# Kernel tuning notes

Measured on AMD Instinct MI355X. Metric: run time of the kernel, lower is better.

Reference implementation:

```python
import jax, jax.numpy as jnp
import numpy as np

H = 4  # attention heads for the single degree-0 fiber

def _layer_norm(x, gamma):
    mu = x.mean(-1, keepdims=True)
    var = ((x - mu) ** 2).mean(-1, keepdims=True)
    return (x - mu) / jnp.sqrt(var + 1e-5) * gamma

def _silu(x):
    return x * jax.nn.sigmoid(x)

def _forward(features, rel_dist, norm_scale, Wq, Wxi, Wxj,
             rp_W1, rp_b1, rp_g1, rp_W2, rp_b2, rp_g2, rp_W3, rp_b3,
             Wkv_out, Wout, neighbor_indices, neighbor_mask):
    b, n, d, _ = features.shape
    k = neighbor_indices.shape[-1]
    hid = Wq.shape[1]
    dh = hid // H
    kvd = Wkv_out.shape[0]
    scale = dh ** -0.5

    # ---- prenorm: RMS (over feature channels) of per-m L2 norms; m=1 for degree 0
    rms = jnp.sqrt(jnp.sum(features ** 2, axis=-2, keepdims=True)) * (d ** -0.5)
    x = features / jnp.maximum(rms, 1e-12) * norm_scale      # (b,n,d,1)
    x = x[..., 0]                                            # (b,n,d)

    # ---- queries
    q = x @ Wq                                               # (b,n,hid)

    # ---- DTP to_kv (degree0->degree0): project xi/xj, gather neighbors, radial kernel
    xi = x @ Wxi
    xj = x @ Wxj
    xg = jax.vmap(lambda t, idx: t[idx])(xj, neighbor_indices)   # (b,n,k,d)
    xe = xg + xi[:, :, None, :]

    hdd = _layer_norm(_silu(rel_dist @ rp_W1 + rp_b1), rp_g1)    # (b,n,k,rh)
    hdd = _layer_norm(_silu(hdd @ rp_W2 + rp_b2), rp_g2)
    R = (hdd @ rp_W3 + rp_b3).reshape(b, n, k, kvd, d)           # per-edge (lo,li) kernel
    kv = jnp.einsum('bnkod,bnkd->bnko', R, xe)                   # (b,n,k,kvd)
    kv = kv @ Wkv_out                                            # DTP project_out
    kk, vv = jnp.split(kv, 2, axis=-1)                           # (b,n,k,hid) each

    # ---- L2-distance attention over neighbors
    qh = q.reshape(b, n, H, dh).transpose(0, 2, 1, 3)            # (b,h,n,dh)
    kh = kk.reshape(b, n, k, H, dh).transpose(0, 3, 1, 2, 4)     # (b,h,n,k,dh)
    vh = vv.reshape(b, n, k, H, dh).transpose(0, 3, 1, 2, 4)
    diff = qh[:, :, :, None, :] - kh + 1e-6                      # F.pairwise_distance eps
    sim = -jnp.sqrt(jnp.sum(diff * diff, axis=-1)) * scale       # (b,h,n,k)
    sim = jnp.where(neighbor_mask[:, None], sim, -jnp.finfo(sim.dtype).max)
    attn = jax.nn.softmax(sim, axis=-1)
    out = jnp.einsum('bhnk,bhnkd->bhnd', attn, vh)
    out = out.transpose(0, 2, 1, 3).reshape(b, n, hid)

    return (out @ Wout)[..., None]                               # (b,n,d,1)

def setup_inputs() -> dict:
    key = jax.random.key(0)
    ks = jax.random.split(key, 16)
    b, n, k, d = 2, 256, 16, 64
    hid = H * 32           # heads * dim_head = 128
    kvd = 2 * hid          # 256
    rh = 64                # radial_hidden_dim
    rnd = lambda i, shape, s=1.0: jax.random.normal(ks[i], shape, jnp.float32) * s
    return dict(
        features=rnd(0, (b, n, d, 1)),
        neighbor_indices=jax.random.randint(ks[1], (b, n, k), 0, n),
        neighbor_mask=jax.random.bernoulli(ks[2], 0.9, (b, n, k)),
        rel_dist=jax.random.uniform(ks[3], (b, n, k, 1), jnp.float32),
        norm_scale=jnp.ones((d, 1), jnp.float32),
        Wq=rnd(4, (d, hid), d ** -0.5),
        Wxi=rnd(5, (d, d), d ** -0.5),
        Wxj=rnd(6, (d, d), d ** -0.5),
        rp_W1=rnd(7, (1, rh)), rp_b1=jnp.zeros((rh,), jnp.float32),
        rp_g1=jnp.ones((rh,), jnp.float32),
        rp_W2=rnd(8, (rh, rh), rh ** -0.5), rp_b2=jnp.zeros((rh,), jnp.float32),
        rp_g2=jnp.ones((rh,), jnp.float32),
        rp_W3=rnd(9, (rh, kvd * d), rh ** -0.5), rp_b3=jnp.zeros((kvd * d,), jnp.float32),
        Wkv_out=rnd(10, (kvd, kvd), kvd ** -0.5),
        Wout=rnd(11, (hid, d), hid ** -0.5),
    )

def reference(features, neighbor_indices, neighbor_mask, rel_dist, norm_scale,
              Wq, Wxi, Wxj, rp_W1, rp_b1, rp_g1, rp_W2, rp_b2, rp_g2,
              rp_W3, rp_b3, Wkv_out, Wout):
    return _forward(features, rel_dist, norm_scale, Wq, Wxi, Wxj,
                    rp_W1, rp_b1, rp_g1, rp_W2, rp_b2, rp_g2, rp_W3, rp_b3,
                    Wkv_out, Wout, neighbor_indices, neighbor_mask)
```

## Files before the change

### kernel.cpp

```cpp
#include <hip/hip_runtime.h>
#include <hip/hip_bf16.h>
#include <float.h>

#define BB 2
#define NN 256
#define DD 64
#define KK 16
#define NH 4
#define HID 128
#define KVD 256
#define RH 64
#define NNODES (BB*NN)
#define NEDGES (NNODES*KK)

typedef unsigned int uint32;
typedef unsigned short ushort_t;
typedef float f32x4_t __attribute__((ext_vector_type(4)));
typedef short bf16x8_t __attribute__((ext_vector_type(8)));
typedef __attribute__((address_space(3))) ushort_t lds_us;
typedef __attribute__((address_space(1))) const ushort_t glb_us;

__device__ __forceinline__ uint32 cvtpk_bf16(float lo, float hi) {
  uint32 r;
  asm("v_cvt_pk_bf16_f32 %0, %1, %2" : "=v"(r) : "v"(lo), "v"(hi));
  return r;
}

__device__ __forceinline__ float wave_sum64(float v) {
  #pragma unroll
  for (int m = 32; m; m >>= 1) v += __shfl_xor(v, m, 64);
  return v;
}

__device__ __forceinline__ ushort_t rne_bf16(float f) {
  uint32 u = __float_as_uint(f);
  return (ushort_t)((u + 0x7FFFu + ((u >> 16) & 1u)) >> 16);
}

__global__ __launch_bounds__(256) void node_w3_kernel(
    const float* __restrict__ feat, const float* __restrict__ gscale,
    const float* __restrict__ Wq, const float* __restrict__ Wxi,
    const float* __restrict__ Wxj,
    const float* __restrict__ W3, const float* __restrict__ b3,
    const float* __restrict__ Wkv,
    float* __restrict__ q_ws, float* __restrict__ xi_ws, float* __restrict__ xj_ws,
    ushort_t* __restrict__ W3bf, ushort_t* __restrict__ Wkvt) {
  int bx = blockIdx.x;
  if (bx >= 648) {
    int i = ((bx - 648) * 256 + threadIdx.x) * 4;
    int n = i >> 8, k0 = i & 255;
    union { uint2 q; ushort_t s[4]; } o;
    #pragma unroll
    for (int j = 0; j < 4; ++j) o.s[j] = rne_bf16(Wkv[(k0 + j) * KVD + n]);
    *(uint2*)(Wkvt + n * KVD + k0) = o.q;
    return;
  }
  if (bx >= 128) {
    const int W3N = 64 * KVD * DD;
    int i = ((bx - 128) * 256 + threadIdx.x) * 8;
    const float* src = (i < W3N) ? (W3 + i) : (b3 + (i - W3N));
    float4 a = ((const float4*)src)[0];
    float4 b = ((const float4*)src)[1];
    float v[8] = {a.x, a.y, a.z, a.w, b.x, b.y, b.z, b.w};
    union { uint4 q; ushort_t s[8]; } o;
    #pragma unroll
    for (int jj = 0; jj < 8; ++jj) o.s[jj] = rne_bf16(v[jj]);
    int rr = i >> 14, j0 = i & 16383;
    int oc = j0 >> 6, gr = (j0 >> 3) & 7;
    int byte_sw = oc * 128 + ((gr * 16) ^ ((oc & 7) << 4));
    *(uint4*)(W3bf + (rr << 14) + (byte_sw >> 1)) = o.q;
    return;
  }
  int sub = threadIdx.x >> 6;
  int t = threadIdx.x & 63;
  int node = bx * 4 + sub;
  __shared__ float xs[4][DD];
  float f = feat[node * DD + t];
  float ss = wave_sum64(f * f);
  float rms = sqrtf(ss) * 0.125f;
  float den = fmaxf(rms, 1e-12f);
  float x = f / den * gscale[t];
  xs[sub][t] = x;
  __syncthreads();
  float q0 = 0.f, q1 = 0.f, xiv = 0.f, xjv = 0.f;
  #pragma unroll 4
  for (int d = 0; d < DD; ++d) {
    float xv = xs[sub][d];
    q0  += xv * Wq[d * HID + t];
    q1  += xv * Wq[d * HID + 64 + t];
    xiv += xv * Wxi[d * DD + t];
    xjv += xv * Wxj[d * DD + t];
  }
  q_ws[node * HID + t] = q0;
  q_ws[node * HID + 64 + t] = q1;
  xi_ws[node * DD + t] = xiv;
  xj_ws[node * DD + t] = xjv;
}

__global__ __launch_bounds__(64) void edge_kernel(
    const int* __restrict__ nbi, const float* __restrict__ rel,
    const float* __restrict__ W1, const float* __restrict__ b1,
    const float* __restrict__ g1, const float* __restrict__ W2,
    const float* __restrict__ b2, const float* __restrict__ g2,
    const float* __restrict__ xi_ws, const float* __restrict__ xj_ws,
    float* __restrict__ h2_ws, float* __restrict__ xe_ws) {
  int e = blockIdx.x;
  int t = threadIdx.x;
  int node = e >> 4;
  int j = e & 15;
  int bb = node >> 8;
  __shared__ float hs[RH];
  float rd = rel[e];
  float h = rd * W1[t] + b1[t];
  h = h / (1.f + expf(-h));
  float mu = wave_sum64(h) * (1.f / RH);
  float c = h - mu;
  float var = wave_sum64(c * c) * (1.f / RH);
  float xn = c * rsqrtf(var + 1e-5f) * g1[t];
  hs[t] = xn;
  __syncthreads();
  float p = b2[t];
  #pragma unroll 4
  for (int r = 0; r < RH; ++r) p += hs[r] * W2[r * RH + t];
  p = p / (1.f + expf(-p));
  mu = wave_sum64(p) * (1.f / RH);
  c = p - mu;
  var = wave_sum64(c * c) * (1.f / RH);
  float h2v = c * rsqrtf(var + 1e-5f) * g2[t];
  h2_ws[e * RH + t] = h2v;
  int nb = nbi[node * KK + j];
  xe_ws[e * DD + t] = xj_ws[(bb * NN + nb) * DD + t] + xi_ws[node * DD + t];
}

#define AFRAG(dst, base, h) {                                     \
  union { bf16x8_t v; uint32 u[4]; } t_;                          \
  t_.u[0] = cvtpk_bf16(xf[(base)+0]*(h), xf[(base)+1]*(h));       \
  t_.u[1] = cvtpk_bf16(xf[(base)+2]*(h), xf[(base)+3]*(h));       \
  t_.u[2] = cvtpk_bf16(xf[(base)+4]*(h), xf[(base)+5]*(h));       \
  t_.u[3] = cvtpk_bf16(xf[(base)+6]*(h), xf[(base)+7]*(h));       \
  dst = t_.v; }

__global__ __launch_bounds__(256) void kv_kernel(
    const ushort_t* __restrict__ W3bf,
    const float* __restrict__ h2_ws, const float* __restrict__ xe_ws,
    float* __restrict__ kv_ws) {
  int bx = blockIdx.x;
  int eb = bx >> 2, ob = bx & 3;
  int o0 = ob * 64;
  int tid = threadIdx.x;
  int we = tid >> 6, l = tid & 63;
  int l15 = l & 15, g = l >> 4;
  int ebase = eb * 64;
  __shared__ float h2_s[64 * 68];
  __shared__ ushort_t bstage[2][2][4096];
  {
    int row = tid >> 2, c0 = (tid & 3) * 16;
    const float* src = h2_ws + (ebase + row) * RH + c0;
    float* dst = &h2_s[row * 68 + c0];
    #pragma unroll
    for (int q = 0; q < 4; ++q) ((float4*)dst)[q] = ((const float4*)src)[q];
  }
  int erow = ebase + we * 16 + l15;
  const float* xsrc = xe_ws + erow * DD + g * 8;
  float xf[16];
  #pragma unroll
  for (int jj = 0; jj < 8; ++jj) { xf[jj] = xsrc[jj]; xf[8 + jj] = xsrc[32 + jj]; }

  #define STAGE(buf, r0_) {                                                   \
    int ra_ = ((r0_) > 64) ? 64 : (r0_);                                      \
    int rb_ = ((r0_) + 1 > 64) ? 64 : ((r0_) + 1);                            \
    const ushort_t* sa_ = W3bf + ((size_t)ra_ << 14) + o0 * 64;               \
    const ushort_t* sb_ = W3bf + ((size_t)rb_ << 14) + o0 * 64;               \
    ushort_t* da_ = &bstage[buf][0][0];                                       \
    ushort_t* db_ = &bstage[buf][1][0];                                       \
    __builtin_amdgcn_global_load_lds((glb_us*)(sa_ + tid * 8),        (lds_us*)(da_ + tid * 8), 16, 0, 0);        \
    __builtin_amdgcn_global_load_lds((glb_us*)(sa_ + 2048 + tid * 8), (lds_us*)(da_ + 2048 + tid * 8), 16, 0, 0); \
    __builtin_amdgcn_global_load_lds((glb_us*)(sb_ + tid * 8),        (lds_us*)(db_ + tid * 8), 16, 0, 0);        \
    __builtin_amdgcn_global_load_lds((glb_us*)(sb_ + 2048 + tid * 8), (lds_us*)(db_ + 2048 + tid * 8), 16, 0, 0); }

  STAGE(0, 0);
  asm volatile("s_waitcnt vmcnt(0)" ::: "memory");
  __syncthreads();

  int e68 = (we * 16 + l15) * 68;
  int swz = (l15 & 7) << 4;
  f32x4_t acc0 = {0,0,0,0}, acc1 = {0,0,0,0}, acc2 = {0,0,0,0}, acc3 = {0,0,0,0};
  int cur = 0;
  for (int p = 0; p < 33; ++p) {
    int r0 = 2 * p;
    if (p < 32) STAGE(cur ^ 1, r0 + 2);
    #pragma unroll
    for (int rl = 0; rl < 2; ++rl) {
      int r = r0 + rl;
      if (r > 64) break;
      const char* bp = (const char*)&bstage[cur][rl][0];
      bf16x8_t bf0 = *(const bf16x8_t*)(bp + l15*128 +    0 + ((g*16)     ^ swz));
      bf16x8_t bf1 = *(const bf16x8_t*)(bp + l15*128 +    0 + (((4+g)*16) ^ swz));
      bf16x8_t bf2 = *(const bf16x8_t*)(bp + l15*128 + 2048 + ((g*16)     ^ swz));
      bf16x8_t bf3 = *(const bf16x8_t*)(bp + l15*128 + 2048 + (((4+g)*16) ^ swz));
      bf16x8_t bf4 = *(const bf16x8_t*)(bp + l15*128 + 4096 + ((g*16)     ^ swz));
      bf16x8_t bf5 = *(const bf16x8_t*)(bp + l15*128 + 4096 + (((4+g)*16) ^ swz));
      bf16x8_t bf6 = *(const bf16x8_t*)(bp + l15*128 + 6144 + ((g*16)     ^ swz));
      bf16x8_t bf7 = *(const bf16x8_t*)(bp + l15*128 + 6144 + (((4+g)*16) ^ swz));
      float h = (r < 64) ? h2_s[e68 + r] : 1.0f;
      bf16x8_t a0, a1;
      AFRAG(a0, 0, h); AFRAG(a1, 8, h);
      acc0 = __builtin_amdgcn_mfma_f32_16x16x32_bf16(a0, bf0, acc0, 0, 0, 0);
      acc0 = __builtin_amdgcn_mfma_f32_16x16x32_bf16(a1, bf1, acc0, 0, 0, 0);
      acc1 = __builtin_amdgcn_mfma_f32_16x16x32_bf16(a0, bf2, acc1, 0, 0, 0);
      acc1 = __builtin_amdgcn_mfma_f32_16x16x32_bf16(a1, bf3, acc1, 0, 0, 0);
      acc2 = __builtin_amdgcn_mfma_f32_16x16x32_bf16(a0, bf4, acc2, 0, 0, 0);
      acc2 = __builtin_amdgcn_mfma_f32_16x16x32_bf16(a1, bf5, acc2, 0, 0, 0);
      acc3 = __builtin_amdgcn_mfma_f32_16x16x32_bf16(a0, bf6, acc3, 0, 0, 0);
      acc3 = __builtin_amdgcn_mfma_f32_16x16x32_bf16(a1, bf7, acc3, 0, 0, 0);
    }
    asm volatile("s_waitcnt vmcnt(0)" ::: "memory");
    __syncthreads();
    cur ^= 1;
  }
  int orow = (ebase + we * 16 + g * 4) * KVD + o0 + l15;
  #pragma unroll
  for (int q = 0; q < 4; ++q) {
    kv_ws[orow + q * KVD +  0] = acc0[q];
    kv_ws[orow + q * KVD + 16] = acc1[q];
    kv_ws[orow + q * KVD + 32] = acc2[q];
    kv_ws[orow + q * KVD + 48] = acc3[q];
  }
}

__global__ __launch_bounds__(128) void attn_kernel(
    const float* __restrict__ q_ws, const float* __restrict__ kv_ws,
    const int* __restrict__ maskp, const ushort_t* __restrict__ Wkvt,
    const float* __restrict__ Wout, float* __restrict__ out) {
  int node = blockIdx.x;
  int tid = threadIdx.x;
  int w = tid >> 6, l = tid & 63;
  int l15 = l & 15, g = l >> 4;
  __shared__ float attn_s[NH * KK];
  __shared__ float o_s[HID];
  bf16x8_t a[8];
  {
    const float* kvrow = kv_ws + (size_t)(node * KK + l15) * KVD + g * 8;
    #pragma unroll
    for (int c = 0; c < 8; ++c) {
      union { bf16x8_t v; uint32 u[4]; } t_;
      t_.u[0] = cvtpk_bf16(kvrow[c*32 + 0], kvrow[c*32 + 1]);
      t_.u[1] = cvtpk_bf16(kvrow[c*32 + 2], kvrow[c*32 + 3]);
      t_.u[2] = cvtpk_bf16(kvrow[c*32 + 4], kvrow[c*32 + 5]);
      t_.u[3] = cvtpk_bf16(kvrow[c*32 + 6], kvrow[c*32 + 7]);
      a[c] = t_.v;
    }
  }
  f32x4_t acc[8];
  #pragma unroll
  for (int nt = 0; nt < 8; ++nt) {
    acc[nt] = (f32x4_t){0.f, 0.f, 0.f, 0.f};
    const ushort_t* bbase = Wkvt + (size_t)(w * 128 + nt * 16 + l15) * KVD + g * 8;
    #pragma unroll
    for (int c = 0; c < 8; ++c) {
      bf16x8_t b = *(const bf16x8_t*)(bbase + c * 32);
      acc[nt] = __builtin_amdgcn_mfma_f32_16x16x32_bf16(a[c], b, acc[nt], 0, 0, 0);
    }
  }
  const float scale = 0.17677669529663689f;
  if (w == 0) {
    float sim[4][4];
    #pragma unroll
    for (int h = 0; h < 4; ++h) {
      #pragma unroll
      for (int q = 0; q < 4; ++q) {
        float s = 0.f;
        #pragma unroll
        for (int p = 0; p < 2; ++p) {
          int nt = h * 2 + p;
          float qv = q_ws[node * HID + nt * 16 + l15];
          float diff = qv - acc[nt][q] + 1e-6f;
          s += diff * diff;
        }
        #pragma unroll
        for (int m = 8; m; m >>= 1) s += __shfl_xor(s, m, 64);
        sim[q][h] = -sqrtf(s) * scale;
      }
    }
    int mv[4];
    #pragma unroll
    for (int q = 0; q < 4; ++q) mv[q] = maskp[node * KK + g * 4 + q];
    #pragma unroll
    for (int h = 0; h < 4; ++h) {
      float sv[4];
      float mx = -FLT_MAX;
      #pragma unroll
      for (int q = 0; q < 4; ++q) {
        sv[q] = mv[q] ? sim[q][h] : -FLT_MAX;
        mx = fmaxf(mx, sv[q]);
      }
      mx = fmaxf(mx, __shfl_xor(mx, 16, 64));
      mx = fmaxf(mx, __shfl_xor(mx, 32, 64));
      float se = 0.f, ev[4];
      #pragma unroll
      for (int q = 0; q < 4; ++q) { ev[q] = expf(sv[q] - mx); se += ev[q]; }
      se += __shfl_xor(se, 16, 64);
      se += __shfl_xor(se, 32, 64);
      float inv = 1.f / se;
      if (l15 == 0) {
        #pragma unroll
        for (int q = 0; q < 4; ++q) attn_s[h * KK + g * 4 + q] = ev[q] * inv;
      }
    }
  }
  __syncthreads();
  if (w == 1) {
    #pragma unroll
    for (int nt = 0; nt < 8; ++nt) {
      int h = nt >> 1;
      float o = 0.f;
      #pragma unroll
      for (int q = 0; q < 4; ++q) o += attn_s[h * KK + g * 4 + q] * acc[nt][q];
      o += __shfl_xor(o, 16, 64);
      o += __shfl_xor(o, 32, 64);
      if (g == 0) o_s[nt * 16 + l15] = o;
    }
  }
  __syncthreads();
  if (tid < DD) {
    float r = 0.f;
    #pragma unroll 4
    for (int cI = 0; cI < HID; ++cI) r += o_s[cI] * Wout[cI * DD + tid];
    out[node * DD + tid] = r;
  }
}

extern "C" void kernel_launch(void* const* d_in, const int* in_sizes, int n_in,
                              void* d_out, int out_size, void* d_ws, size_t ws_size,
                              hipStream_t stream) {
  const float* feat = (const float*)d_in[0];
  const int*   nbi  = (const int*)d_in[1];
  const int*   msk  = (const int*)d_in[2];
  const float* rel  = (const float*)d_in[3];
  const float* gsc  = (const float*)d_in[4];
  const float* Wq   = (const float*)d_in[5];
  const float* Wxi  = (const float*)d_in[6];
  const float* Wxj  = (const float*)d_in[7];
  const float* W1   = (const float*)d_in[8];
  const float* b1   = (const float*)d_in[9];
  const float* g1   = (const float*)d_in[10];
  const float* W2   = (const float*)d_in[11];
  const float* b2   = (const float*)d_in[12];
  const float* g2   = (const float*)d_in[13];
  const float* W3   = (const float*)d_in[14];
  const float* b3   = (const float*)d_in[15];
  const float* Wkv  = (const float*)d_in[16];
  const float* Wout = (const float*)d_in[17];

  float* ws      = (float*)d_ws;
  float* q_ws    = ws;
  float* xi_ws   = q_ws  + NNODES * HID;
  float* xj_ws   = xi_ws + NNODES * DD;
  float* h2_ws   = xj_ws + NNODES * DD;
  float* xe_ws   = h2_ws + NEDGES * RH;
  float* kv_ws   = xe_ws + NEDGES * DD;
  ushort_t* W3bf = (ushort_t*)(kv_ws + NEDGES * KVD);
  ushort_t* Wkvt = W3bf + 65 * 16384;

  node_w3_kernel<<<712, 256, 0, stream>>>(feat, gsc, Wq, Wxi, Wxj, W3, b3, Wkv,
                                          q_ws, xi_ws, xj_ws, W3bf, Wkvt);
  edge_kernel<<<NEDGES, 64, 0, stream>>>(nbi, rel, W1, b1, g1, W2, b2, g2,
                                         xi_ws, xj_ws, h2_ws, xe_ws);
  kv_kernel<<<512, 256, 0, stream>>>(W3bf, h2_ws, xe_ws, kv_ws);
  attn_kernel<<<NNODES, 128, 0, stream>>>(q_ws, kv_ws, msk, Wkvt, Wout,
                                          (float*)d_out);
}
```

Before: 164.2 us.

## Fuse edge MLP, radial-kernel MFMA contraction and attention into one kernel

```diff
diff --git a/kernel.cpp b/kernel.cpp
--- a/kernel.cpp
+++ b/kernel.cpp
@@ -97,157 +97,160 @@
   xj_ws[node * DD + t] = xjv;
 }
 
-__global__ __launch_bounds__(64) void edge_kernel(
+#define AFRAG(dst, arr, base, h) {                                \
+  union { bf16x8_t v; uint32 u[4]; } t_;                          \
+  t_.u[0] = cvtpk_bf16(arr[(base)+0]*(h), arr[(base)+1]*(h));     \
+  t_.u[1] = cvtpk_bf16(arr[(base)+2]*(h), arr[(base)+3]*(h));     \
+  t_.u[2] = cvtpk_bf16(arr[(base)+4]*(h), arr[(base)+5]*(h));     \
+  t_.u[3] = cvtpk_bf16(arr[(base)+6]*(h), arr[(base)+7]*(h));     \
+  dst = t_.v; }
+
+#define STAGE2(buf, rr) {                                                      \
+  const ushort_t* s_ = W3bf + ((size_t)(rr) << 14);                            \
+  ushort_t* d_ = &bstage[buf][0];                                              \
+  __builtin_amdgcn_global_load_lds((glb_us*)(s_ + tid * 8),         (lds_us*)(d_ + tid * 8),         16, 0, 0); \
+  __builtin_amdgcn_global_load_lds((glb_us*)(s_ + 2048  + tid * 8), (lds_us*)(d_ + 2048  + tid * 8), 16, 0, 0); \
+  __builtin_amdgcn_global_load_lds((glb_us*)(s_ + 4096  + tid * 8), (lds_us*)(d_ + 4096  + tid * 8), 16, 0, 0); \
+  __builtin_amdgcn_global_load_lds((glb_us*)(s_ + 6144  + tid * 8), (lds_us*)(d_ + 6144  + tid * 8), 16, 0, 0); \
+  __builtin_amdgcn_global_load_lds((glb_us*)(s_ + 8192  + tid * 8), (lds_us*)(d_ + 8192  + tid * 8), 16, 0, 0); \
+  __builtin_amdgcn_global_load_lds((glb_us*)(s_ + 10240 + tid * 8), (lds_us*)(d_ + 10240 + tid * 8), 16, 0, 0); \
+  __builtin_amdgcn_global_load_lds((glb_us*)(s_ + 12288 + tid * 8), (lds_us*)(d_ + 12288 + tid * 8), 16, 0, 0); \
+  __builtin_amdgcn_global_load_lds((glb_us*)(s_ + 14336 + tid * 8), (lds_us*)(d_ + 14336 + tid * 8), 16, 0, 0); }
+
+__global__ __launch_bounds__(256, 1) void fused_kernel(
     const int* __restrict__ nbi, const float* __restrict__ rel,
     const float* __restrict__ W1, const float* __restrict__ b1,
     const float* __restrict__ g1, const float* __restrict__ W2,
     const float* __restrict__ b2, const float* __restrict__ g2,
     const float* __restrict__ xi_ws, const float* __restrict__ xj_ws,
-    float* __restrict__ h2_ws, float* __restrict__ xe_ws) {
-  int e = blockIdx.x;
-  int t = threadIdx.x;
-  int node = e >> 4;
-  int j = e & 15;
-  int bb = node >> 8;
-  __shared__ float hs[RH];
-  float rd = rel[e];
-  float h = rd * W1[t] + b1[t];
-  h = h / (1.f + expf(-h));
-  float mu = wave_sum64(h) * (1.f / RH);
-  float c = h - mu;
-  float var = wave_sum64(c * c) * (1.f / RH);
-  float xn = c * rsqrtf(var + 1e-5f) * g1[t];
-  hs[t] = xn;
-  __syncthreads();
-  float p = b2[t];
-  #pragma unroll 4
-  for (int r = 0; r < RH; ++r) p += hs[r] * W2[r * RH + t];
-  p = p / (1.f + expf(-p));
-  mu = wave_sum64(p) * (1.f / RH);
-  c = p - mu;
-  var = wave_sum64(c * c) * (1.f / RH);
-  float h2v = c * rsqrtf(var + 1e-5f) * g2[t];
-  h2_ws[e * RH + t] = h2v;
-  int nb = nbi[node * KK + j];
-  xe_ws[e * DD + t] = xj_ws[(bb * NN + nb) * DD + t] + xi_ws[node * DD + t];
-}
-
-#define AFRAG(dst, base, h) {                                     \
-  union { bf16x8_t v; uint32 u[4]; } t_;                          \
-  t_.u[0] = cvtpk_bf16(xf[(base)+0]*(h), xf[(base)+1]*(h));       \
-  t_.u[1] = cvtpk_bf16(xf[(base)+2]*(h), xf[(base)+3]*(h));       \
-  t_.u[2] = cvtpk_bf16(xf[(base)+4]*(h), xf[(base)+5]*(h));       \
-  t_.u[3] = cvtpk_bf16(xf[(base)+6]*(h), xf[(base)+7]*(h));       \
-  dst = t_.v; }
-
-__global__ __launch_bounds__(256) void kv_kernel(
-    const ushort_t* __restrict__ W3bf,
-    const float* __restrict__ h2_ws, const float* __restrict__ xe_ws,
-    float* __restrict__ kv_ws) {
-  int bx = blockIdx.x;
-  int eb = bx >> 2, ob = bx & 3;
-  int o0 = ob * 64;
+    const ushort_t* __restrict__ W3bf, const ushort_t* __restrict__ Wkvt,
+    const float* __restrict__ q_ws, const int* __restrict__ maskp,
+    const float* __restrict__ Wout, float* __restrict__ out) {
+  int b = blockIdx.x;
   int tid = threadIdx.x;
-  int we = tid >> 6, l = tid & 63;
+  int wv = tid >> 6, l = tid & 63;
   int l15 = l & 15, g = l >> 4;
-  int ebase = eb * 64;
-  __shared__ float h2_s[64 * 68];
-  __shared__ ushort_t bstage[2][2][4096];
+
+  __shared__ ushort_t bstage[2][16384];
+  __shared__ float h2_s[32 * 68];
+  __shared__ float xe_s[32 * 68];
+  __shared__ float attn_s[2][NH * KK];
+  __shared__ float o_s[2][HID];
+
+  STAGE2(0, 0);
+
   {
-    int row = tid >> 2, c0 = (tid & 3) * 16;
-    const float* src = h2_ws + (ebase + row) * RH + c0;
-    float* dst = &h2_s[row * 68 + c0];
-    #pragma unroll
-    for (int q = 0; q < 4; ++q) ((float4*)dst)[q] = ((const float4*)src)[q];
-  }
-  int erow = ebase + we * 16 + l15;
-  const float* xsrc = xe_ws + erow * DD + g * 8;
-  float xf[16];
+    float w1r = W1[l], b1r = b1[l], g1r = g1[l];
+    float b2r = b2[l], g2r = g2[l];
+    float w2r[64];
+    #pragma unroll
+    for (int r = 0; r < 64; ++r) w2r[r] = W2[r * RH + l];
+    int node_w = b * 2 + (wv >> 1);
+    int bbn = node_w >> 8;
+    float xir = xi_ws[node_w * DD + l];
+    for (int i = 0; i < 8; ++i) {
+      int e_loc = wv * 8 + i;
+      float rd = rel[b * 32 + e_loc];
+      float h = rd * w1r + b1r;
+      h = h / (1.f + expf(-h));
+      float mu = wave_sum64(h) * (1.f / RH);
+      float c = h - mu;
+      float var = wave_sum64(c * c) * (1.f / RH);
+      float xn = c * rsqrtf(var + 1e-5f) * g1r;
+      float p = b2r;
+      #pragma unroll
+      for (int r = 0; r < 64; ++r) {
+        float s = __uint_as_float(__builtin_amdgcn_readlane(__float_as_uint(xn), r));
+        p += s * w2r[r];
+      }
+      p = p / (1.f + expf(-p));
+      mu = wave_sum64(p) * (1.f / RH);
+      c = p - mu;
+      var = wave_sum64(c * c) * (1.f / RH);
+      float h2v = c * rsqrtf(var + 1e-5f) * g2r;
+      h2_s[e_loc * 68 + l] = h2v;
+      int nb = nbi[node_w * KK + (e_loc & 15)];
+      xe_s[e_loc * 68 + l] = xj_ws[(bbn * NN + nb) * DD + l] + xir;
+    }
+  }
+  asm volatile("s_waitcnt vmcnt(0)" ::: "memory");
+  __syncthreads();
+
+  float xfA[16], xfB[16];
   #pragma unroll
-  for (int jj = 0; jj < 8; ++jj) { xf[jj] = xsrc[jj]; xf[8 + jj] = xsrc[32 + jj]; }
-
-  #define STAGE(buf, r0_) {                                                   \
-    int ra_ = ((r0_) > 64) ? 64 : (r0_);                                      \
-    int rb_ = ((r0_) + 1 > 64) ? 64 : ((r0_) + 1);                            \
-    const ushort_t* sa_ = W3bf + ((size_t)ra_ << 14) + o0 * 64;               \
-    const ushort_t* sb_ = W3bf + ((size_t)rb_ << 14) + o0 * 64;               \
-    ushort_t* da_ = &bstage[buf][0][0];                                       \
-    ushort_t* db_ = &bstage[buf][1][0];                                       \
-    __builtin_amdgcn_global_load_lds((glb_us*)(sa_ + tid * 8),        (lds_us*)(da_ + tid * 8), 16, 0, 0);        \
-    __builtin_amdgcn_global_load_lds((glb_us*)(sa_ + 2048 + tid * 8), (lds_us*)(da_ + 2048 + tid * 8), 16, 0, 0); \
-    __builtin_amdgcn_global_load_lds((glb_us*)(sb_ + tid * 8),        (lds_us*)(db_ + tid * 8), 16, 0, 0);        \
-    __builtin_amdgcn_global_load_lds((glb_us*)(sb_ + 2048 + tid * 8), (lds_us*)(db_ + 2048 + tid * 8), 16, 0, 0); }
-
-  STAGE(0, 0);
-  asm volatile("s_waitcnt vmcnt(0)" ::: "memory");
-  __syncthreads();
-
-  int e68 = (we * 16 + l15) * 68;
+  for (int j = 0; j < 8; ++j) {
+    xfA[j]     = xe_s[l15 * 68 + g * 8 + j];
+    xfA[8 + j] = xe_s[l15 * 68 + 32 + g * 8 + j];
+    xfB[j]     = xe_s[(16 + l15) * 68 + g * 8 + j];
+    xfB[8 + j] = xe_s[(16 + l15) * 68 + 32 + g * 8 + j];
+  }
   int swz = (l15 & 7) << 4;
-  f32x4_t acc0 = {0,0,0,0}, acc1 = {0,0,0,0}, acc2 = {0,0,0,0}, acc3 = {0,0,0,0};
+  f32x4_t accA[4], accB[4];
+  #pragma unroll
+  for (int oi = 0; oi < 4; ++oi) {
+    accA[oi] = (f32x4_t){0.f, 0.f, 0.f, 0.f};
+    accB[oi] = (f32x4_t){0.f, 0.f, 0.f, 0.f};
+  }
   int cur = 0;
-  for (int p = 0; p < 33; ++p) {
-    int r0 = 2 * p;
-    if (p < 32) STAGE(cur ^ 1, r0 + 2);
-    #pragma unroll
-    for (int rl = 0; rl < 2; ++rl) {
-      int r = r0 + rl;
-      if (r > 64) break;
-      const char* bp = (const char*)&bstage[cur][rl][0];
-      bf16x8_t bf0 = *(const bf16x8_t*)(bp + l15*128 +    0 + ((g*16)     ^ swz));
-      bf16x8_t bf1 = *(const bf16x8_t*)(bp + l15*128 +    0 + (((4+g)*16) ^ swz));
-      bf16x8_t bf2 = *(const bf16x8_t*)(bp + l15*128 + 2048 + ((g*16)     ^ swz));
-      bf16x8_t bf3 = *(const bf16x8_t*)(bp + l15*128 + 2048 + (((4+g)*16) ^ swz));
-      bf16x8_t bf4 = *(const bf16x8_t*)(bp + l15*128 + 4096 + ((g*16)     ^ swz));
-      bf16x8_t bf5 = *(const bf16x8_t*)(bp + l15*128 + 4096 + (((4+g)*16) ^ swz));
-      bf16x8_t bf6 = *(const bf16x8_t*)(bp + l15*128 + 6144 + ((g*16)     ^ swz));
-      bf16x8_t bf7 = *(const bf16x8_t*)(bp + l15*128 + 6144 + (((4+g)*16) ^ swz));
-      float h = (r < 64) ? h2_s[e68 + r] : 1.0f;
-      bf16x8_t a0, a1;
-      AFRAG(a0, 0, h); AFRAG(a1, 8, h);
-      acc0 = __builtin_amdgcn_mfma_f32_16x16x32_bf16(a0, bf0, acc0, 0, 0, 0);
-      acc0 = __builtin_amdgcn_mfma_f32_16x16x32_bf16(a1, bf1, acc0, 0, 0, 0);
-      acc1 = __builtin_amdgcn_mfma_f32_16x16x32_bf16(a0, bf2, acc1, 0, 0, 0);
-      acc1 = __builtin_amdgcn_mfma_f32_16x16x32_bf16(a1, bf3, acc1, 0, 0, 0);
-      acc2 = __builtin_amdgcn_mfma_f32_16x16x32_bf16(a0, bf4, acc2, 0, 0, 0);
-      acc2 = __builtin_amdgcn_mfma_f32_16x16x32_bf16(a1, bf5, acc2, 0, 0, 0);
-      acc3 = __builtin_amdgcn_mfma_f32_16x16x32_bf16(a0, bf6, acc3, 0, 0, 0);
-      acc3 = __builtin_amdgcn_mfma_f32_16x16x32_bf16(a1, bf7, acc3, 0, 0, 0);
+  for (int p = 0; p <= 64; ++p) {
+    if (p < 64) STAGE2(cur ^ 1, p + 1);
+    float hA = (p < 64) ? h2_s[l15 * 68 + p] : 1.0f;
+    float hB = (p < 64) ? h2_s[(16 + l15) * 68 + p] : 1.0f;
+    bf16x8_t a0A, a1A, a0B, a1B;
+    AFRAG(a0A, xfA, 0, hA); AFRAG(a1A, xfA, 8, hA);
+    AFRAG(a0B, xfB, 0, hB); AFRAG(a1B, xfB, 8, hB);
+    const char* bp = (const char*)&bstage[cur][0] + wv * 8192 + l15 * 128;
+    #pragma unroll
+    for (int oi = 0; oi < 4; ++oi) {
+      bf16x8_t bv0 = *(const bf16x8_t*)(bp + oi * 2048 + ((g * 16) ^ swz));
+      bf16x8_t bv1 = *(const bf16x8_t*)(bp + oi * 2048 + (((4 + g) * 16) ^ swz));
+      accA[oi] = __builtin_amdgcn_mfma_f32_16x16x32_bf16(a0A, bv0, accA[oi], 0, 0, 0);
+      accA[oi] = __builtin_amdgcn_mfma_f32_16x16x32_bf16(a1A, bv1, accA[oi], 0, 0, 0);
+      accB[oi] = __builtin_amdgcn_mfma_f32_16x16x32_bf16(a0B, bv0, accB[oi], 0, 0, 0);
+      accB[oi] = __builtin_amdgcn_mfma_f32_16x16x32_bf16(a1B, bv1, accB[oi], 0, 0, 0);
     }
     asm volatile("s_waitcnt vmcnt(0)" ::: "memory");
     __syncthreads();
     cur ^= 1;
   }
-  int orow = (ebase + we * 16 + g * 4) * KVD + o0 + l15;
-  #pragma unroll
-  for (int q = 0; q < 4; ++q) {
-    kv_ws[orow + q * KVD +  0] = acc0[q];
-    kv_ws[orow + q * KVD + 16] = acc1[q];
-    kv_ws[orow + q * KVD + 32] = acc2[q];
-    kv_ws[orow + q * KVD + 48] = acc3[q];
-  }
-}
-
-__global__ __launch_bounds__(128) void attn_kernel(
-    const float* __restrict__ q_ws, const float* __restrict__ kv_ws,
-    const int* __restrict__ maskp, const ushort_t* __restrict__ Wkvt,
-    const float* __restrict__ Wout, float* __restrict__ out) {
-  int node = blockIdx.x;
-  int tid = threadIdx.x;
-  int w = tid >> 6, l = tid & 63;
-  int l15 = l & 15, g = l >> 4;
-  __shared__ float attn_s[NH * KK];
-  __shared__ float o_s[HID];
+
+  float* kvf = (float*)&bstage[0][0];
+  {
+    #pragma unroll
+    for (int m = 0; m < 2; ++m) {
+      #pragma unroll
+      for (int oi = 0; oi < 4; ++oi) {
+        f32x4_t av = m ? accB[oi] : accA[oi];
+        int f = wv * 64 + oi * 16 + l15;
+        int fu = f >> 2, fl = f & 3;
+        #pragma unroll
+        for (int q = 0; q < 4; ++q) {
+          int e = m * 16 + g * 4 + q;
+          kvf[e * 256 + ((fu ^ (e & 7)) << 2) + fl] = av[q];
+        }
+      }
+    }
+  }
+  __syncthreads();
+
+  int role = wv & 1, nl = wv >> 1;
+  int node = b * 2 + nl;
   bf16x8_t a[8];
   {
-    const float* kvrow = kv_ws + (size_t)(node * KK + l15) * KVD + g * 8;
+    int e = nl * 16 + l15;
+    const float* kr = kvf + e * 256;
+    int sw = l15 & 7;
     #pragma unroll
     for (int c = 0; c < 8; ++c) {
+      int u0 = (c * 8 + g * 2) ^ sw;
+      int u1 = (c * 8 + g * 2 + 1) ^ sw;
+      f32x4_t v0 = *(const f32x4_t*)(kr + u0 * 4);
+      f32x4_t v1 = *(const f32x4_t*)(kr + u1 * 4);
       union { bf16x8_t v; uint32 u[4]; } t_;
-      t_.u[0] = cvtpk_bf16(kvrow[c*32 + 0], kvrow[c*32 + 1]);
-      t_.u[1] = cvtpk_bf16(kvrow[c*32 + 2], kvrow[c*32 + 3]);
-      t_.u[2] = cvtpk_bf16(kvrow[c*32 + 4], kvrow[c*32 + 5]);
-      t_.u[3] = cvtpk_bf16(kvrow[c*32 + 6], kvrow[c*32 + 7]);
+      t_.u[0] = cvtpk_bf16(v0.x, v0.y);
+      t_.u[1] = cvtpk_bf16(v0.z, v0.w);
+      t_.u[2] = cvtpk_bf16(v1.x, v1.y);
+      t_.u[3] = cvtpk_bf16(v1.z, v1.w);
       a[c] = t_.v;
     }
   }
@@ -255,15 +258,15 @@
   #pragma unroll
   for (int nt = 0; nt < 8; ++nt) {
     acc[nt] = (f32x4_t){0.f, 0.f, 0.f, 0.f};
-    const ushort_t* bbase = Wkvt + (size_t)(w * 128 + nt * 16 + l15) * KVD + g * 8;
+    const ushort_t* bbase = Wkvt + (size_t)(role * 128 + nt * 16 + l15) * KVD + g * 8;
     #pragma unroll
     for (int c = 0; c < 8; ++c) {
-      bf16x8_t b = *(const bf16x8_t*)(bbase + c * 32);
-      acc[nt] = __builtin_amdgcn_mfma_f32_16x16x32_bf16(a[c], b, acc[nt], 0, 0, 0);
+      bf16x8_t bv = *(const bf16x8_t*)(bbase + c * 32);
+      acc[nt] = __builtin_amdgcn_mfma_f32_16x16x32_bf16(a[c], bv, acc[nt], 0, 0, 0);
     }
   }
   const float scale = 0.17677669529663689f;
-  if (w == 0) {
+  if (role == 0) {
     float sim[4][4];
     #pragma unroll
     for (int h = 0; h < 4; ++h) {
@@ -271,8 +274,8 @@
       for (int q = 0; q < 4; ++q) {
         float s = 0.f;
         #pragma unroll
-        for (int p = 0; p < 2; ++p) {
-          int nt = h * 2 + p;
+        for (int pq = 0; pq < 2; ++pq) {
+          int nt = h * 2 + pq;
           float qv = q_ws[node * HID + nt * 16 + l15];
           float diff = qv - acc[nt][q] + 1e-6f;
           s += diff * diff;
@@ -304,29 +307,30 @@
       float inv = 1.f / se;
       if (l15 == 0) {
         #pragma unroll
-        for (int q = 0; q < 4; ++q) attn_s[h * KK + g * 4 + q] = ev[q] * inv;
-      }
-    }
-  }
-  __syncthreads();
-  if (w == 1) {
+        for (int q = 0; q < 4; ++q) attn_s[nl][h * KK + g * 4 + q] = ev[q] * inv;
+      }
+    }
+  }
+  __syncthreads();
+  if (role == 1) {
     #pragma unroll
     for (int nt = 0; nt < 8; ++nt) {
       int h = nt >> 1;
       float o = 0.f;
       #pragma unroll
-      for (int q = 0; q < 4; ++q) o += attn_s[h * KK + g * 4 + q] * acc[nt][q];
+      for (int q = 0; q < 4; ++q) o += attn_s[nl][h * KK + g * 4 + q] * acc[nt][q];
       o += __shfl_xor(o, 16, 64);
       o += __shfl_xor(o, 32, 64);
-      if (g == 0) o_s[nt * 16 + l15] = o;
-    }
-  }
-  __syncthreads();
-  if (tid < DD) {
+      if (g == 0) o_s[nl][nt * 16 + l15] = o;
+    }
+  }
+  __syncthreads();
+  if (tid < 128) {
+    int n2 = tid >> 6, t = tid & 63;
     float r = 0.f;
     #pragma unroll 4
-    for (int cI = 0; cI < HID; ++cI) r += o_s[cI] * Wout[cI * DD + tid];
-    out[node * DD + tid] = r;
+    for (int cI = 0; cI < HID; ++cI) r += o_s[n2][cI] * Wout[cI * DD + t];
+    out[(b * 2 + n2) * DD + t] = r;
   }
 }
 
@@ -356,17 +360,12 @@
   float* q_ws    = ws;
   float* xi_ws   = q_ws  + NNODES * HID;
   float* xj_ws   = xi_ws + NNODES * DD;
-  float* h2_ws   = xj_ws + NNODES * DD;
-  float* xe_ws   = h2_ws + NEDGES * RH;
-  float* kv_ws   = xe_ws + NEDGES * DD;
-  ushort_t* W3bf = (ushort_t*)(kv_ws + NEDGES * KVD);
+  ushort_t* W3bf = (ushort_t*)(xj_ws + NNODES * DD);
   ushort_t* Wkvt = W3bf + 65 * 16384;
 
   node_w3_kernel<<<712, 256, 0, stream>>>(feat, gsc, Wq, Wxi, Wxj, W3, b3, Wkv,
                                           q_ws, xi_ws, xj_ws, W3bf, Wkvt);
-  edge_kernel<<<NEDGES, 64, 0, stream>>>(nbi, rel, W1, b1, g1, W2, b2, g2,
-                                         xi_ws, xj_ws, h2_ws, xe_ws);
-  kv_kernel<<<512, 256, 0, stream>>>(W3bf, h2_ws, xe_ws, kv_ws);
-  attn_kernel<<<NNODES, 128, 0, stream>>>(q_ws, kv_ws, msk, Wkvt, Wout,
-                                          (float*)d_out);
-}
+  fused_kernel<<<256, 256, 0, stream>>>(nbi, rel, W1, b1, g1, W2, b2, g2,
+                                        xi_ws, xj_ws, W3bf, Wkvt,
+                                        q_ws, msk, Wout, (float*)d_out);
+}
```

New measurement: 189.9 us. 15.7% more time.
